# Performance work log

Measured on AMD Instinct MI355X. Metric: run time of the kernel, lower is better.

## Reference

```python
import jax, jax.numpy as jnp
import numpy as np

N, E, G = 50000, 400000, 64          # nodes, edges, graphs in batch
IN_DIM, OUT_DIM = 64, 128
N_ETYPES, N_STEPS = 4, 8


def setup_inputs() -> dict:
    key = jax.random.key(0)
    ks = jax.random.split(key, 13)
    s = 1.0 / np.sqrt(OUT_DIM)
    u = lambda k, shp: jax.random.uniform(k, shp, jnp.float32, -s, s)
    return {
        "node_features": jax.random.normal(ks[0], (N, IN_DIM), jnp.float32),
        "src": jax.random.randint(ks[1], (E,), 0, N),
        "dst": jax.random.randint(ks[2], (E,), 0, N),
        "etype": jax.random.randint(ks[3], (E,), 0, N_ETYPES),
        "graph_ids": jax.random.randint(ks[4], (N,), 0, G),
        "Ws": u(ks[5], (N_ETYPES, OUT_DIM, OUT_DIM)),   # per-edge-type linear
        "bs": u(ks[6], (N_ETYPES, OUT_DIM)),
        "W_ih": u(ks[7], (3 * OUT_DIM, OUT_DIM)),        # GRUCell (r,z,n order)
        "W_hh": u(ks[8], (3 * OUT_DIM, OUT_DIM)),
        "b_ih": u(ks[9], (3 * OUT_DIM,)),
        "b_hh": u(ks[10], (3 * OUT_DIM,)),
        "W_cls": u(ks[11], (1, OUT_DIM + IN_DIM)),
        "b_cls": u(ks[12], (1,)),
    }


def _gru_cell(x, h, W_ih, W_hh, b_ih, b_hh):
    gi = x @ W_ih.T + b_ih
    gh = h @ W_hh.T + b_hh
    ir, iz, i_n = jnp.split(gi, 3, axis=-1)
    hr, hz, h_n = jnp.split(gh, 3, axis=-1)
    r = jax.nn.sigmoid(ir + hr)
    z = jax.nn.sigmoid(iz + hz)
    n = jnp.tanh(i_n + r * h_n)
    return (1.0 - z) * n + z * h


def reference(node_features, src, dst, etype, graph_ids,
              Ws, bs, W_ih, W_hh, b_ih, b_hh, W_cls, b_cls):
    # pad input features to OUT_DIM (GGNN.forward zero_pad)
    h = jnp.concatenate(
        [node_features, jnp.zeros((N, OUT_DIM - IN_DIM), node_features.dtype)], -1)

    def step(h, _):
        # per-edge-type linear transform of all node states: (T, N, D)
        Wh = jnp.einsum('nd,tkd->tnk', h, Ws) + bs[:, None, :]
        msg = Wh[etype, src]                                  # (E, D) gather
        a = jax.ops.segment_sum(msg, dst, num_segments=N)     # scatter-add
        return _gru_cell(a, h, W_ih, W_hh, b_ih, b_hh), None

    h, _ = jax.lax.scan(step, h, None, length=N_STEPS)

    hcat = jnp.concatenate([h, node_features], -1)            # (N, OUT+IN)
    feats = jax.ops.segment_sum(hcat, graph_ids, num_segments=G)  # sum readout
    return jax.nn.sigmoid(feats @ W_cls.T + b_cls)            # (G, 1)
```

## Files before the change

kernel.cpp:

```cpp
#include <hip/hip_runtime.h>
#include <hip/hip_bf16.h>
#include <math.h>


#define NN 50000
#define NE 400000
#define NG 64
#define IND 64
#define OD 128
#define NN4 (NN * 4)
#define RC 8

typedef _Float16 f16x8 __attribute__((ext_vector_type(8)));
typedef _Float16 f16x4 __attribute__((ext_vector_type(4)));
typedef _Float16 f16x2 __attribute__((ext_vector_type(2)));
typedef float f32x4 __attribute__((ext_vector_type(4)));

__device__ inline unsigned short f2h(float x) {
    _Float16 hv = (_Float16)x;
    unsigned short u;
    __builtin_memcpy(&u, &hv, 2);
    return u;
}

__global__ void k_cvtws(const float* __restrict__ Ws, unsigned short* __restrict__ Wcat) {
    int i = blockIdx.x * 256 + threadIdx.x;
    if (i >= 65536) return;
    int o = i >> 9, col = i & 511;
    int t = col >> 7, k = col & 127;
    Wcat[i] = f2h(Ws[t * 16384 + o * 128 + k]);
}

__global__ void k_pack(const float* __restrict__ Wih, const float* __restrict__ Whh,
                       const float* __restrict__ bih, const float* __restrict__ bhh,
                       unsigned short* __restrict__ Wpk, float* __restrict__ bpk) {
    int i = blockIdx.x * 256 + threadIdx.x;
    if (i < 98304) {
        int c = i >> 14, j = i & 16383, o = j >> 7, k = j & 127;
        const float* W = (c & 1) ? Whh : Wih;
        Wpk[i] = f2h(W[((c >> 1) * 128 + o) * 128 + k]);
    }
    if (i < 512) {
        float b;
        if (i < 256) b = bih[i] + bhh[i];
        else if (i < 384) b = bih[i];
        else b = bhh[i - 128];
        bpk[i] = b;
    }
}

__global__ void k_init_h(const float* __restrict__ nf, float* __restrict__ h,
                         unsigned short* __restrict__ hx) {
    int i = blockIdx.x * 256 + threadIdx.x;
    if (i >= NN * OD) return;
    int n = i >> 7, d = i & 127;
    float v = (d < IND) ? nf[n * IND + d] : 0.f;
    h[i] = v;
    hx[(size_t)n * 256 + 128 + d] = f2h(v);
}

__global__ void k_count(const int* __restrict__ dst, const int* __restrict__ et,
                        int* __restrict__ deg4) {
    int e = blockIdx.x * 256 + threadIdx.x;
    if (e < NE) atomicAdd(&deg4[dst[e] * 4 + et[e]], 1);
}

__global__ void k_scan1(const int* __restrict__ deg, int* __restrict__ rowp,
                        int* __restrict__ bsum, int n) {
    __shared__ int buf[1024];
    int tid = threadIdx.x;
    int i = blockIdx.x * 1024 + tid;
    int v = (i < n) ? deg[i] : 0;
    buf[tid] = v;
    __syncthreads();
    for (int off = 1; off < 1024; off <<= 1) {
        int t = (tid >= off) ? buf[tid - off] : 0;
        __syncthreads();
        buf[tid] += t;
        __syncthreads();
    }
    if (i < n) rowp[i + 1] = buf[tid];
    if (tid == 1023) bsum[blockIdx.x] = buf[tid];
}

__global__ void k_scan2(int* __restrict__ bsum, int nb) {
    __shared__ int buf[256];
    int tid = threadIdx.x;
    int v = (tid < nb) ? bsum[tid] : 0;
    buf[tid] = v;
    __syncthreads();
    for (int off = 1; off < 256; off <<= 1) {
        int t = (tid >= off) ? buf[tid - off] : 0;
        __syncthreads();
        buf[tid] += t;
        __syncthreads();
    }
    if (tid < nb) bsum[tid] = buf[tid] - v;
}

__global__ void k_scan3(const int* __restrict__ deg, const int* __restrict__ bsum,
                        int* __restrict__ rowp, int* __restrict__ cursor, int n) {
    int i = blockIdx.x * 256 + threadIdx.x;
    if (i >= n) return;
    int incl = rowp[i + 1] + bsum[i >> 10];
    rowp[i + 1] = incl;
    cursor[i] = incl - deg[i];
    if (i == 0) rowp[0] = 0;
}

__global__ void k_fill(const int* __restrict__ src, const int* __restrict__ dst,
                       const int* __restrict__ et, int* __restrict__ cursor,
                       int* __restrict__ epk) {
    int e = blockIdx.x * 256 + threadIdx.x;
    if (e < NE) {
        int t = et[e];
        int pos = atomicAdd(&cursor[dst[e] * 4 + t], 1);
        epk[pos] = src[e] | (t << 16);
    }
}

__global__ void k_gcount(const int* __restrict__ gid, int* __restrict__ gdeg) {
    __shared__ int c[NG];
    int tid = threadIdx.x;
    if (tid < NG) c[tid] = 0;
    __syncthreads();
    int n = blockIdx.x * 1024 + tid;
    if (n < NN) atomicAdd(&c[gid[n]], 1);
    __syncthreads();
    if (tid < NG && c[tid] > 0) atomicAdd(&gdeg[tid], c[tid]);
}

__global__ void k_gscan(const int* __restrict__ gdeg, int* __restrict__ growp,
                        int* __restrict__ gcur) {
    __shared__ int buf[NG];
    int tid = threadIdx.x;
    int v = gdeg[tid];
    buf[tid] = v;
    __syncthreads();
    for (int off = 1; off < NG; off <<= 1) {
        int t = (tid >= off) ? buf[tid - off] : 0;
        __syncthreads();
        buf[tid] += t;
        __syncthreads();
    }
    growp[tid + 1] = buf[tid];
    gcur[tid] = buf[tid] - v;
    if (tid == 0) growp[0] = 0;
}

__global__ void k_gfill(const int* __restrict__ gid, int* __restrict__ gcur,
                        int* __restrict__ nlist) {
    __shared__ int lcnt[NG];
    __shared__ int lbase[NG];
    int tid = threadIdx.x;
    if (tid < NG) lcnt[tid] = 0;
    __syncthreads();
    int n = blockIdx.x * 1024 + tid;
    int g = -1, rank = 0;
    if (n < NN) { g = gid[n]; rank = atomicAdd(&lcnt[g], 1); }
    __syncthreads();
    if (tid < NG && lcnt[tid] > 0) lbase[tid] = atomicAdd(&gcur[tid], lcnt[tid]);
    __syncthreads();
    if (n < NN) nlist[lbase[g] + rank] = n;
}

__global__ __launch_bounds__(256) void k_agg_gemm(
    const unsigned short* __restrict__ hx,
    const int* __restrict__ rowp4, const int* __restrict__ epk,
    const int* __restrict__ deg4,
    const unsigned short* __restrict__ Wcat,
    const float* __restrict__ bs,
    unsigned short* __restrict__ hxw) {
    __shared__ unsigned short Sh[4 * 32 * 136];
    __shared__ float Bsb[512];

    const int tid = threadIdx.x;
    const int m0 = blockIdx.x * 32;

    Bsb[tid] = bs[tid];
    Bsb[tid + 256] = bs[tid + 256];

    const int r = tid >> 3;
    const int sl = tid & 7;
    const int d0 = sl * 16;
    const int n = m0 + r;

    float a0[16], a1[16], a2[16], a3[16];
#pragma unroll
    for (int k = 0; k < 16; ++k) { a0[k] = 0.f; a1[k] = 0.f; a2[k] = 0.f; a3[k] = 0.f; }

    if (n < NN) {
        int i = rowp4[n * 4], end = rowp4[n * 4 + 4];
        for (; i + 2 <= end; i += 2) {
            int p0 = epk[i], p1 = epk[i + 1];
            const f16x8* r0 = (const f16x8*)&hx[(size_t)(p0 & 0xFFFF) * 256 + 128 + d0];
            const f16x8* r1 = (const f16x8*)&hx[(size_t)(p1 & 0xFFFF) * 256 + 128 + d0];
            f16x8 u0 = r0[0], u1 = r0[1];
            f16x8 v0 = r1[0], v1 = r1[1];
            int e0 = p0 >> 16, e1 = p1 >> 16;
#pragma unroll
            for (int k = 0; k < 8; ++k) {
                float f0 = (float)u0[k], f1 = (float)u1[k];
                float g0 = (float)v0[k], g1 = (float)v1[k];
                a0[k]     += (e0 == 0 ? f0 : 0.f) + (e1 == 0 ? g0 : 0.f);
                a0[8 + k] += (e0 == 0 ? f1 : 0.f) + (e1 == 0 ? g1 : 0.f);
                a1[k]     += (e0 == 1 ? f0 : 0.f) + (e1 == 1 ? g0 : 0.f);
                a1[8 + k] += (e0 == 1 ? f1 : 0.f) + (e1 == 1 ? g1 : 0.f);
                a2[k]     += (e0 == 2 ? f0 : 0.f) + (e1 == 2 ? g0 : 0.f);
                a2[8 + k] += (e0 == 2 ? f1 : 0.f) + (e1 == 2 ? g1 : 0.f);
                a3[k]     += (e0 == 3 ? f0 : 0.f) + (e1 == 3 ? g0 : 0.f);
                a3[8 + k] += (e0 == 3 ? f1 : 0.f) + (e1 == 3 ? g1 : 0.f);
            }
        }
        if (i < end) {
            int p0 = epk[i];
            const f16x8* r0 = (const f16x8*)&hx[(size_t)(p0 & 0xFFFF) * 256 + 128 + d0];
            f16x8 u0 = r0[0], u1 = r0[1];
            int e0 = p0 >> 16;
#pragma unroll
            for (int k = 0; k < 8; ++k) {
                float f0 = (float)u0[k], f1 = (float)u1[k];
                a0[k] += (e0 == 0 ? f0 : 0.f); a0[8 + k] += (e0 == 0 ? f1 : 0.f);
                a1[k] += (e0 == 1 ? f0 : 0.f); a1[8 + k] += (e0 == 1 ? f1 : 0.f);
                a2[k] += (e0 == 2 ? f0 : 0.f); a2[8 + k] += (e0 == 2 ? f1 : 0.f);
                a3[k] += (e0 == 3 ? f0 : 0.f); a3[8 + k] += (e0 == 3 ? f1 : 0.f);
            }
        }
    }

    {
        f16x8 w0, w1;
#pragma unroll
        for (int k = 0; k < 8; ++k) { w0[k] = (_Float16)a0[k]; w1[k] = (_Float16)a0[8 + k]; }
        *(f16x8*)&Sh[0 * 4352 + r * 136 + d0] = w0; *(f16x8*)&Sh[0 * 4352 + r * 136 + d0 + 8] = w1;
#pragma unroll
        for (int k = 0; k < 8; ++k) { w0[k] = (_Float16)a1[k]; w1[k] = (_Float16)a1[8 + k]; }
        *(f16x8*)&Sh[1 * 4352 + r * 136 + d0] = w0; *(f16x8*)&Sh[1 * 4352 + r * 136 + d0 + 8] = w1;
#pragma unroll
        for (int k = 0; k < 8; ++k) { w0[k] = (_Float16)a2[k]; w1[k] = (_Float16)a2[8 + k]; }
        *(f16x8*)&Sh[2 * 4352 + r * 136 + d0] = w0; *(f16x8*)&Sh[2 * 4352 + r * 136 + d0 + 8] = w1;
#pragma unroll
        for (int k = 0; k < 8; ++k) { w0[k] = (_Float16)a3[k]; w1[k] = (_Float16)a3[8 + k]; }
        *(f16x8*)&Sh[3 * 4352 + r * 136 + d0] = w0; *(f16x8*)&Sh[3 * 4352 + r * 136 + d0 + 8] = w1;
    }
    __syncthreads();

    const int lane = tid & 63;
    const int w = tid >> 6;
    const int lr = lane & 15;
    const int q = lane >> 4;
    const int rt = w >> 1;
    const int cts = (w & 1) * 4;

    f32x4 acc[4];
#pragma unroll
    for (int j = 0; j < 4; ++j) acc[j] = (f32x4){0.f, 0.f, 0.f, 0.f};

#pragma unroll
    for (int ks = 0; ks < 16; ++ks) {
        int t = ks >> 2, ksl = ks & 3;
        f16x8 af = *(const f16x8*)&Sh[t * 4352 + (rt * 16 + lr) * 136 + ksl * 32 + q * 8];
#pragma unroll
        for (int j = 0; j < 4; ++j) {
            f16x8 bf = *(const f16x8*)&Wcat[((cts + j) * 16 + lr) * 512 + ks * 32 + q * 8];
            acc[j] = __builtin_amdgcn_mfma_f32_16x16x32_f16(af, bf, acc[j], 0, 0, 0);
        }
    }

    int rowbase = m0 + rt * 16 + q * 4;
#pragma unroll
    for (int rr = 0; rr < 4; ++rr) {
        int n2 = rowbase + rr;
        if (n2 < NN) {
            int4 c = *(const int4*)&deg4[n2 * 4];
            unsigned short* arow = hxw + (size_t)n2 * 256;
#pragma unroll
            for (int j = 0; j < 4; ++j) {
                int col = (cts + j) * 16 + lr;
                float v = acc[j][rr]
                        + c.x * Bsb[col] + c.y * Bsb[128 + col]
                        + c.z * Bsb[256 + col] + c.w * Bsb[384 + col];
                arow[col] = f2h(v);
            }
        }
    }
}

__global__ __launch_bounds__(512) void k_gates_gru(
    const unsigned short* __restrict__ hx,
    const unsigned short* __restrict__ Wpk,
    const float* __restrict__ bpk,
    float* __restrict__ h,
    unsigned short* __restrict__ hxw) {
    __shared__ unsigned short As[64 * 264];
    __shared__ unsigned short Bs[128 * 136];
    __shared__ float Bsb[512];

    const int tid = threadIdx.x;
    const int m0 = blockIdx.x * 64;

    Bsb[tid] = bpk[tid];

    const uint4* H4 = (const uint4*)hx;
#pragma unroll
    for (int it = 0; it < 4; ++it) {
        int i = tid + it * 512;
        int row = i >> 5, qq = i & 31;
        int nn = m0 + row;
        uint4 v = (nn < NN) ? H4[(size_t)nn * 32 + qq] : make_uint4(0u, 0u, 0u, 0u);
        *(uint4*)&As[row * 264 + qq * 8] = v;
    }

    const int lane = tid & 63;
    const int w = tid >> 6;
    const int lr = lane & 15;
    const int q = lane >> 4;
    const int rt = w >> 1;
    const int cts = (w & 1) * 4;

    const uint4* W4 = (const uint4*)Wpk;

    f32x4 accR[4], accZ[4], accI[4], accH[4];
#pragma unroll
    for (int j = 0; j < 4; ++j) {
        accR[j] = (f32x4){0.f, 0.f, 0.f, 0.f};
        accZ[j] = (f32x4){0.f, 0.f, 0.f, 0.f};
        accI[j] = (f32x4){0.f, 0.f, 0.f, 0.f};
        accH[j] = (f32x4){0.f, 0.f, 0.f, 0.f};
    }

#define GCHUNK(C, ACC)                                                              \
    __syncthreads();                                                                \
    _Pragma("unroll")                                                               \
    for (int it = 0; it < 4; ++it) {                                                \
        int i = tid + it * 512;                                                     \
        *(uint4*)&Bs[(i >> 4) * 136 + (i & 15) * 8] = W4[(C) * 2048 + i];           \
    }                                                                               \
    __syncthreads();                                                                \
    _Pragma("unroll")                                                               \
    for (int ks = 0; ks < 4; ++ks) {                                                \
        f16x8 af = *(const f16x8*)&As[(rt * 16 + lr) * 264 + ((C) & 1) * 128        \
                                      + ks * 32 + q * 8];                           \
        _Pragma("unroll")                                                           \
        for (int j = 0; j < 4; ++j) {                                               \
            f16x8 bf = *(const f16x8*)&Bs[((cts + j) * 16 + lr) * 136               \
                                          + ks * 32 + q * 8];                       \
            ACC[j] = __builtin_amdgcn_mfma_f32_16x16x32_f16(af, bf, ACC[j], 0, 0, 0); \
        }                                                                           \
    }

    GCHUNK(0, accR)
    GCHUNK(1, accR)
    GCHUNK(2, accZ)
    GCHUNK(3, accZ)
    GCHUNK(4, accI)
    GCHUNK(5, accH)
#undef GCHUNK

    int rowb = m0 + rt * 16 + q * 4;
#pragma unroll
    for (int rr = 0; rr < 4; ++rr) {
        int n2 = rowb + rr;
        if (n2 < NN) {
            float* hrow = h + (size_t)n2 * OD;
            unsigned short* hbrow = hxw + (size_t)n2 * 256 + 128;
#pragma unroll
            for (int j = 0; j < 4; ++j) {
                int col = (cts + j) * 16 + lr;
                float R = 1.f / (1.f + __expf(-(accR[j][rr] + Bsb[col])));
                float Z = 1.f / (1.f + __expf(-(accZ[j][rr] + Bsb[128 + col])));
                float NV = tanhf(accI[j][rr] + Bsb[256 + col]
                                 + R * (accH[j][rr] + Bsb[384 + col]));
                float hold = hrow[col];
                float hnew = (1.f - Z) * NV + Z * hold;
                hrow[col] = hnew;
                hbrow[col] = f2h(hnew);
            }
        }
    }
}

__global__ void k_readout(const float* __restrict__ h, const float* __restrict__ nf,
                          const int* __restrict__ nlist, const int* __restrict__ growp,
                          float* __restrict__ partial) {
    int g = blockIdx.x >> 3, c = blockIdx.x & (RC - 1);
    int d = threadIdx.x;
    int s = growp[g], e = growp[g + 1], len = e - s;
    int i0 = s + (int)((long long)len * c / RC);
    int i1 = s + (int)((long long)len * (c + 1) / RC);
    float acc = 0.f;
    for (int i = i0; i < i1; ++i) {
        int n = nlist[i];
        acc += (d < OD) ? h[(size_t)n * OD + d] : nf[(size_t)n * IND + (d - OD)];
    }
    partial[(size_t)blockIdx.x * 192 + d] = acc;
}

__global__ void k_reduce(const float* __restrict__ partial, float* __restrict__ feats) {
    int i = blockIdx.x * 256 + threadIdx.x;
    if (i >= NG * 192) return;
    int g = i / 192, d = i % 192;
    float s = 0.f;
    for (int c = 0; c < RC; ++c) s += partial[(size_t)(g * RC + c) * 192 + d];
    feats[i] = s;
}

__global__ void k_final(const float* __restrict__ feats, const float* __restrict__ W_cls,
                        const float* __restrict__ b_cls, float* __restrict__ out) {
    int g = threadIdx.x;
    if (g >= NG) return;
    float acc = b_cls[0];
    for (int d = 0; d < 192; ++d) acc += feats[g * 192 + d] * W_cls[d];
    out[g] = 1.f / (1.f + __expf(-acc));
}

extern "C" void kernel_launch(void* const* d_in, const int* in_sizes, int n_in,
                              void* d_out, int out_size, void* d_ws, size_t ws_size,
                              hipStream_t stream) {
    const float* nf    = (const float*)d_in[0];
    const int*   src   = (const int*)d_in[1];
    const int*   dst   = (const int*)d_in[2];
    const int*   et    = (const int*)d_in[3];
    const int*   gid   = (const int*)d_in[4];
    const float* Ws    = (const float*)d_in[5];
    const float* bs    = (const float*)d_in[6];
    const float* W_ih  = (const float*)d_in[7];
    const float* W_hh  = (const float*)d_in[8];
    const float* b_ih  = (const float*)d_in[9];
    const float* b_hh  = (const float*)d_in[10];
    const float* W_cls = (const float*)d_in[11];
    const float* b_cls = (const float*)d_in[12];
    float* out = (float*)d_out;

    char* ws = (char*)d_ws;
    size_t off = 0;
    auto alloc = [&](size_t bytes) -> void* {
        off = (off + 255) & ~(size_t)255;
        void* p = ws + off;
        off += bytes;
        return p;
    };
    float*          h    = (float*)alloc((size_t)NN * OD * 4);
    unsigned short* hx   = (unsigned short*)alloc((size_t)NN * 256 * 2);
    int*   deg4    = (int*)alloc((size_t)NN4 * 4);
    int*   rowp4   = (int*)alloc((size_t)(NN4 + 1) * 4);
    int*   cursor4 = (int*)alloc((size_t)NN4 * 4);
    int*   epk     = (int*)alloc((size_t)NE * 4);
    int*   bsum    = (int*)alloc(256 * 4);
    int*   gdeg    = (int*)alloc(NG * 4);
    int*   growp   = (int*)alloc((NG + 1) * 4);
    int*   gcur    = (int*)alloc(NG * 4);
    int*   nlist   = (int*)alloc((size_t)NN * 4);
    float* feats   = (float*)alloc((size_t)NG * 192 * 4);
    float* partial = (float*)alloc((size_t)NG * RC * 192 * 4);
    unsigned short* Wcat = (unsigned short*)alloc((size_t)65536 * 2);
    unsigned short* Wpk  = (unsigned short*)alloc((size_t)98304 * 2);
    float*          bpk  = (float*)alloc(512 * 4);
    (void)ws_size; (void)in_sizes; (void)n_in; (void)out_size;

    hipMemsetAsync(deg4, 0, (size_t)NN4 * 4, stream);
    hipMemsetAsync(gdeg, 0, NG * 4, stream);

    k_cvtws<<<(65536 + 255) / 256, 256, 0, stream>>>(Ws, Wcat);
    k_pack<<<(98304 + 255) / 256, 256, 0, stream>>>(W_ih, W_hh, b_ih, b_hh, Wpk, bpk);

    k_init_h<<<(NN * OD + 255) / 256, 256, 0, stream>>>(nf, h, hx);

    k_count<<<(NE + 255) / 256, 256, 0, stream>>>(dst, et, deg4);
    const int nb4 = (NN4 + 1023) / 1024;
    k_scan1<<<nb4, 1024, 0, stream>>>(deg4, rowp4, bsum, NN4);
    k_scan2<<<1, 256, 0, stream>>>(bsum, nb4);
    k_scan3<<<(NN4 + 255) / 256, 256, 0, stream>>>(deg4, bsum, rowp4, cursor4, NN4);
    k_fill<<<(NE + 255) / 256, 256, 0, stream>>>(src, dst, et, cursor4, epk);

    const int nbn = (NN + 1023) / 1024;
    k_gcount<<<nbn, 1024, 0, stream>>>(gid, gdeg);
    k_gscan<<<1, NG, 0, stream>>>(gdeg, growp, gcur);
    k_gfill<<<nbn, 1024, 0, stream>>>(gid, gcur, nlist);

    const int mt32 = (NN + 31) / 32;
    const int mt64 = (NN + 63) / 64;
    for (int s = 0; s < 8; ++s) {
        k_agg_gemm<<<mt32, 256, 0, stream>>>(hx, rowp4, epk, deg4, Wcat, bs, hx);
        k_gates_gru<<<mt64, 512, 0, stream>>>(hx, Wpk, bpk, h, hx);
    }

    k_readout<<<NG * RC, 192, 0, stream>>>(h, nf, nlist, growp, partial);
    k_reduce<<<(NG * 192 + 255) / 256, 256, 0, stream>>>(partial, feats);
    k_final<<<1, 64, 0, stream>>>(feats, W_cls, b_cls, out);
}
```

Measured before the change: 1.133 ms.

## Gather edges wave-per-8-nodes with segmented accumulation keyed by packed dst/type

```diff
diff --git a/kernel.cpp b/kernel.cpp
--- a/kernel.cpp
+++ b/kernel.cpp
@@ -114,8 +114,9 @@
     int e = blockIdx.x * 256 + threadIdx.x;
     if (e < NE) {
         int t = et[e];
-        int pos = atomicAdd(&cursor[dst[e] * 4 + t], 1);
-        epk[pos] = src[e] | (t << 16);
+        int d = dst[e];
+        int pos = atomicAdd(&cursor[d * 4 + t], 1);
+        epk[pos] = src[e] | (t << 16) | ((d & 31) << 18);
     }
 }
 
@@ -176,81 +177,77 @@
 
     const int tid = threadIdx.x;
     const int m0 = blockIdx.x * 32;
+    const int wv = tid >> 6;
+    const int lane = tid & 63;
 
     Bsb[tid] = bs[tid];
     Bsb[tid + 256] = bs[tid + 256];
-
-    const int r = tid >> 3;
-    const int sl = tid & 7;
-    const int d0 = sl * 16;
-    const int n = m0 + r;
-
-    float a0[16], a1[16], a2[16], a3[16];
-#pragma unroll
-    for (int k = 0; k < 16; ++k) { a0[k] = 0.f; a1[k] = 0.f; a2[k] = 0.f; a3[k] = 0.f; }
-
-    if (n < NN) {
-        int i = rowp4[n * 4], end = rowp4[n * 4 + 4];
-        for (; i + 2 <= end; i += 2) {
-            int p0 = epk[i], p1 = epk[i + 1];
-            const f16x8* r0 = (const f16x8*)&hx[(size_t)(p0 & 0xFFFF) * 256 + 128 + d0];
-            const f16x8* r1 = (const f16x8*)&hx[(size_t)(p1 & 0xFFFF) * 256 + 128 + d0];
-            f16x8 u0 = r0[0], u1 = r0[1];
-            f16x8 v0 = r1[0], v1 = r1[1];
-            int e0 = p0 >> 16, e1 = p1 >> 16;
-#pragma unroll
-            for (int k = 0; k < 8; ++k) {
-                float f0 = (float)u0[k], f1 = (float)u1[k];
-                float g0 = (float)v0[k], g1 = (float)v1[k];
-                a0[k]     += (e0 == 0 ? f0 : 0.f) + (e1 == 0 ? g0 : 0.f);
-                a0[8 + k] += (e0 == 0 ? f1 : 0.f) + (e1 == 0 ? g1 : 0.f);
-                a1[k]     += (e0 == 1 ? f0 : 0.f) + (e1 == 1 ? g0 : 0.f);
-                a1[8 + k] += (e0 == 1 ? f1 : 0.f) + (e1 == 1 ? g1 : 0.f);
-                a2[k]     += (e0 == 2 ? f0 : 0.f) + (e1 == 2 ? g0 : 0.f);
-                a2[8 + k] += (e0 == 2 ? f1 : 0.f) + (e1 == 2 ? g1 : 0.f);
-                a3[k]     += (e0 == 3 ? f0 : 0.f) + (e1 == 3 ? g0 : 0.f);
-                a3[8 + k] += (e0 == 3 ? f1 : 0.f) + (e1 == 3 ? g1 : 0.f);
+    {
+        unsigned int* z = (unsigned int*)Sh;
+#pragma unroll
+        for (int i = tid; i < 8704; i += 256) z[i] = 0u;
+    }
+    __syncthreads();
+
+    {
+        const int d2 = lane * 2;
+        int n0 = m0 + wv * 8; if (n0 > NN) n0 = NN;
+        int n1 = n0 + 8;      if (n1 > NN) n1 = NN;
+        const int ebeg = rowp4[n0 * 4];
+        const int eend = rowp4[n1 * 4];
+
+        float a0 = 0.f, a1 = 0.f;
+        int cur = -1;
+        int kq[8];
+        int base = ebeg;
+#pragma unroll
+        for (int j = 0; j < 8; ++j) kq[j] = (base + j < eend) ? epk[base + j] : -1;
+        while (base < eend) {
+            const int nb2 = base + 8;
+            f16x2 v[8];
+#pragma unroll
+            for (int j = 0; j < 8; ++j) {
+                int p = kq[j];
+                if (p >= 0)
+                    v[j] = *(const f16x2*)&hx[(size_t)(p & 0xFFFF) * 256 + 128 + d2];
+                else {
+                    v[j][0] = (_Float16)0.f; v[j][1] = (_Float16)0.f;
+                }
             }
+            int kn[8];
+#pragma unroll
+            for (int j = 0; j < 8; ++j) kn[j] = (nb2 + j < eend) ? epk[nb2 + j] : -1;
+#pragma unroll
+            for (int j = 0; j < 8; ++j) {
+                int p = kq[j];
+                if (p >= 0) {
+                    int key = p >> 16;
+                    if (key != cur) {
+                        if (cur >= 0) {
+                            f16x2 fv; fv[0] = (_Float16)a0; fv[1] = (_Float16)a1;
+                            *(f16x2*)&Sh[(cur & 3) * 4352 + (cur >> 2) * 136 + d2] = fv;
+                        }
+                        cur = key; a0 = 0.f; a1 = 0.f;
+                    }
+                    a0 += (float)v[j][0];
+                    a1 += (float)v[j][1];
+                }
+            }
+#pragma unroll
+            for (int j = 0; j < 8; ++j) kq[j] = kn[j];
+            base = nb2;
         }
-        if (i < end) {
-            int p0 = epk[i];
-            const f16x8* r0 = (const f16x8*)&hx[(size_t)(p0 & 0xFFFF) * 256 + 128 + d0];
-            f16x8 u0 = r0[0], u1 = r0[1];
-            int e0 = p0 >> 16;
-#pragma unroll
-            for (int k = 0; k < 8; ++k) {
-                float f0 = (float)u0[k], f1 = (float)u1[k];
-                a0[k] += (e0 == 0 ? f0 : 0.f); a0[8 + k] += (e0 == 0 ? f1 : 0.f);
-                a1[k] += (e0 == 1 ? f0 : 0.f); a1[8 + k] += (e0 == 1 ? f1 : 0.f);
-                a2[k] += (e0 == 2 ? f0 : 0.f); a2[8 + k] += (e0 == 2 ? f1 : 0.f);
-                a3[k] += (e0 == 3 ? f0 : 0.f); a3[8 + k] += (e0 == 3 ? f1 : 0.f);
-            }
+        if (cur >= 0) {
+            f16x2 fv; fv[0] = (_Float16)a0; fv[1] = (_Float16)a1;
+            *(f16x2*)&Sh[(cur & 3) * 4352 + (cur >> 2) * 136 + d2] = fv;
         }
     }
-
-    {
-        f16x8 w0, w1;
-#pragma unroll
-        for (int k = 0; k < 8; ++k) { w0[k] = (_Float16)a0[k]; w1[k] = (_Float16)a0[8 + k]; }
-        *(f16x8*)&Sh[0 * 4352 + r * 136 + d0] = w0; *(f16x8*)&Sh[0 * 4352 + r * 136 + d0 + 8] = w1;
-#pragma unroll
-        for (int k = 0; k < 8; ++k) { w0[k] = (_Float16)a1[k]; w1[k] = (_Float16)a1[8 + k]; }
-        *(f16x8*)&Sh[1 * 4352 + r * 136 + d0] = w0; *(f16x8*)&Sh[1 * 4352 + r * 136 + d0 + 8] = w1;
-#pragma unroll
-        for (int k = 0; k < 8; ++k) { w0[k] = (_Float16)a2[k]; w1[k] = (_Float16)a2[8 + k]; }
-        *(f16x8*)&Sh[2 * 4352 + r * 136 + d0] = w0; *(f16x8*)&Sh[2 * 4352 + r * 136 + d0 + 8] = w1;
-#pragma unroll
-        for (int k = 0; k < 8; ++k) { w0[k] = (_Float16)a3[k]; w1[k] = (_Float16)a3[8 + k]; }
-        *(f16x8*)&Sh[3 * 4352 + r * 136 + d0] = w0; *(f16x8*)&Sh[3 * 4352 + r * 136 + d0 + 8] = w1;
-    }
-    __syncthreads();
-
-    const int lane = tid & 63;
-    const int w = tid >> 6;
+    __syncthreads();
+
     const int lr = lane & 15;
     const int q = lane >> 4;
-    const int rt = w >> 1;
-    const int cts = (w & 1) * 4;
+    const int rt = wv >> 1;
+    const int cts = (wv & 1) * 4;
 
     f32x4 acc[4];
 #pragma unroll
```

New measurement: 1.203 ms. 6.2% more time.

## Fuse aggregation GEMM and GRU gate kernels into one step kernel with ping-pong buffers

Applied to the files above, without the earlier changes.

```diff
diff --git a/kernel.cpp b/kernel.cpp
--- a/kernel.cpp
+++ b/kernel.cpp
@@ -50,13 +50,13 @@
 }
 
 __global__ void k_init_h(const float* __restrict__ nf, float* __restrict__ h,
-                         unsigned short* __restrict__ hx) {
+                         unsigned short* __restrict__ hb0) {
     int i = blockIdx.x * 256 + threadIdx.x;
     if (i >= NN * OD) return;
     int n = i >> 7, d = i & 127;
     float v = (d < IND) ? nf[n * IND + d] : 0.f;
     h[i] = v;
-    hx[(size_t)n * 256 + 128 + d] = f2h(v);
+    hb0[i] = f2h(v);
 }
 
 __global__ void k_count(const int* __restrict__ dst, const int* __restrict__ et,
@@ -164,21 +164,33 @@
     if (n < NN) nlist[lbase[g] + rank] = n;
 }
 
-__global__ __launch_bounds__(256) void k_agg_gemm(
-    const unsigned short* __restrict__ hx,
+__global__ __launch_bounds__(256) void k_step(
+    const unsigned short* __restrict__ hbc,
+    unsigned short* __restrict__ hbn,
+    float* __restrict__ h,
     const int* __restrict__ rowp4, const int* __restrict__ epk,
     const int* __restrict__ deg4,
     const unsigned short* __restrict__ Wcat,
     const float* __restrict__ bs,
-    unsigned short* __restrict__ hxw) {
+    const unsigned short* __restrict__ Wpk,
+    const float* __restrict__ bpk) {
     __shared__ unsigned short Sh[4 * 32 * 136];
-    __shared__ float Bsb[512];
+    __shared__ unsigned short As[32 * 264];
 
     const int tid = threadIdx.x;
     const int m0 = blockIdx.x * 32;
 
-    Bsb[tid] = bs[tid];
-    Bsb[tid + 256] = bs[tid + 256];
+    {
+        const uint4* Hb4 = (const uint4*)hbc;
+#pragma unroll
+        for (int it = 0; it < 2; ++it) {
+            int i = tid + it * 256;
+            int row = i >> 4, qq = i & 15;
+            int nn = m0 + row;
+            uint4 v = (nn < NN) ? Hb4[(size_t)nn * 16 + qq] : make_uint4(0u, 0u, 0u, 0u);
+            *(uint4*)&As[row * 264 + 128 + qq * 8] = v;
+        }
+    }
 
     const int r = tid >> 3;
     const int sl = tid & 7;
@@ -193,8 +205,8 @@
         int i = rowp4[n * 4], end = rowp4[n * 4 + 4];
         for (; i + 2 <= end; i += 2) {
             int p0 = epk[i], p1 = epk[i + 1];
-            const f16x8* r0 = (const f16x8*)&hx[(size_t)(p0 & 0xFFFF) * 256 + 128 + d0];
-            const f16x8* r1 = (const f16x8*)&hx[(size_t)(p1 & 0xFFFF) * 256 + 128 + d0];
+            const f16x8* r0 = (const f16x8*)&hbc[(size_t)(p0 & 0xFFFF) * 128 + d0];
+            const f16x8* r1 = (const f16x8*)&hbc[(size_t)(p1 & 0xFFFF) * 128 + d0];
             f16x8 u0 = r0[0], u1 = r0[1];
             f16x8 v0 = r1[0], v1 = r1[1];
             int e0 = p0 >> 16, e1 = p1 >> 16;
@@ -214,7 +226,7 @@
         }
         if (i < end) {
             int p0 = epk[i];
-            const f16x8* r0 = (const f16x8*)&hx[(size_t)(p0 & 0xFFFF) * 256 + 128 + d0];
+            const f16x8* r0 = (const f16x8*)&hbc[(size_t)(p0 & 0xFFFF) * 128 + d0];
             f16x8 u0 = r0[0], u1 = r0[1];
             int e0 = p0 >> 16;
 #pragma unroll
@@ -249,75 +261,49 @@
     const int w = tid >> 6;
     const int lr = lane & 15;
     const int q = lane >> 4;
-    const int rt = w >> 1;
-    const int cts = (w & 1) * 4;
-
-    f32x4 acc[4];
-#pragma unroll
-    for (int j = 0; j < 4; ++j) acc[j] = (f32x4){0.f, 0.f, 0.f, 0.f};
-
-#pragma unroll
-    for (int ks = 0; ks < 16; ++ks) {
-        int t = ks >> 2, ksl = ks & 3;
-        f16x8 af = *(const f16x8*)&Sh[t * 4352 + (rt * 16 + lr) * 136 + ksl * 32 + q * 8];
-#pragma unroll
-        for (int j = 0; j < 4; ++j) {
-            f16x8 bf = *(const f16x8*)&Wcat[((cts + j) * 16 + lr) * 512 + ks * 32 + q * 8];
-            acc[j] = __builtin_amdgcn_mfma_f32_16x16x32_f16(af, bf, acc[j], 0, 0, 0);
-        }
-    }
-
-    int rowbase = m0 + rt * 16 + q * 4;
-#pragma unroll
-    for (int rr = 0; rr < 4; ++rr) {
-        int n2 = rowbase + rr;
-        if (n2 < NN) {
-            int4 c = *(const int4*)&deg4[n2 * 4];
-            unsigned short* arow = hxw + (size_t)n2 * 256;
+    const int rt = w & 1;
+    const int cts = (w >> 1) * 4;
+
+    {
+        f32x4 acc[4];
+#pragma unroll
+        for (int j = 0; j < 4; ++j) acc[j] = (f32x4){0.f, 0.f, 0.f, 0.f};
+
+#pragma unroll
+        for (int ks = 0; ks < 16; ++ks) {
+            int t = ks >> 2, ksl = ks & 3;
+            f16x8 af = *(const f16x8*)&Sh[t * 4352 + (rt * 16 + lr) * 136 + ksl * 32 + q * 8];
 #pragma unroll
             for (int j = 0; j < 4; ++j) {
-                int col = (cts + j) * 16 + lr;
-                float v = acc[j][rr]
-                        + c.x * Bsb[col] + c.y * Bsb[128 + col]
-                        + c.z * Bsb[256 + col] + c.w * Bsb[384 + col];
-                arow[col] = f2h(v);
+                f16x8 bf = *(const f16x8*)&Wcat[((cts + j) * 16 + lr) * 512 + ks * 32 + q * 8];
+                acc[j] = __builtin_amdgcn_mfma_f32_16x16x32_f16(af, bf, acc[j], 0, 0, 0);
             }
         }
-    }
-}
-
-__global__ __launch_bounds__(512) void k_gates_gru(
-    const unsigned short* __restrict__ hx,
-    const unsigned short* __restrict__ Wpk,
-    const float* __restrict__ bpk,
-    float* __restrict__ h,
-    unsigned short* __restrict__ hxw) {
-    __shared__ unsigned short As[64 * 264];
-    __shared__ unsigned short Bs[128 * 136];
-    __shared__ float Bsb[512];
-
-    const int tid = threadIdx.x;
-    const int m0 = blockIdx.x * 64;
-
-    Bsb[tid] = bpk[tid];
-
-    const uint4* H4 = (const uint4*)hx;
-#pragma unroll
-    for (int it = 0; it < 4; ++it) {
-        int i = tid + it * 512;
-        int row = i >> 5, qq = i & 31;
-        int nn = m0 + row;
-        uint4 v = (nn < NN) ? H4[(size_t)nn * 32 + qq] : make_uint4(0u, 0u, 0u, 0u);
-        *(uint4*)&As[row * 264 + qq * 8] = v;
-    }
-
-    const int lane = tid & 63;
-    const int w = tid >> 6;
-    const int lr = lane & 15;
-    const int q = lane >> 4;
-    const int rt = w >> 1;
-    const int cts = (w & 1) * 4;
-
+
+        int rowb = rt * 16 + q * 4;
+#pragma unroll
+        for (int rr = 0; rr < 4; ++rr) {
+            int rl = rowb + rr;
+            int n2 = m0 + rl;
+            if (n2 < NN) {
+                int4 c = *(const int4*)&deg4[n2 * 4];
+#pragma unroll
+                for (int j = 0; j < 4; ++j) {
+                    int col = (cts + j) * 16 + lr;
+                    float v = acc[j][rr]
+                            + c.x * bs[col] + c.y * bs[128 + col]
+                            + c.z * bs[256 + col] + c.w * bs[384 + col];
+                    As[rl * 264 + col] = f2h(v);
+                }
+            } else {
+#pragma unroll
+                for (int j = 0; j < 4; ++j)
+                    As[rl * 264 + (cts + j) * 16 + lr] = 0;
+            }
+        }
+    }
+
+    unsigned short* Bs = Sh;
     const uint4* W4 = (const uint4*)Wpk;
 
     f32x4 accR[4], accZ[4], accI[4], accH[4];
@@ -332,8 +318,8 @@
 #define GCHUNK(C, ACC)                                                              \
     __syncthreads();                                                                \
     _Pragma("unroll")                                                               \
-    for (int it = 0; it < 4; ++it) {                                                \
-        int i = tid + it * 512;                                                     \
+    for (int it = 0; it < 8; ++it) {                                                \
+        int i = tid + it * 256;                                                     \
         *(uint4*)&Bs[(i >> 4) * 136 + (i & 15) * 8] = W4[(C) * 2048 + i];           \
     }                                                                               \
     __syncthreads();                                                                \
@@ -363,14 +349,14 @@
         int n2 = rowb + rr;
         if (n2 < NN) {
             float* hrow = h + (size_t)n2 * OD;
-            unsigned short* hbrow = hxw + (size_t)n2 * 256 + 128;
+            unsigned short* hbrow = hbn + (size_t)n2 * OD;
 #pragma unroll
             for (int j = 0; j < 4; ++j) {
                 int col = (cts + j) * 16 + lr;
-                float R = 1.f / (1.f + __expf(-(accR[j][rr] + Bsb[col])));
-                float Z = 1.f / (1.f + __expf(-(accZ[j][rr] + Bsb[128 + col])));
-                float NV = tanhf(accI[j][rr] + Bsb[256 + col]
-                                 + R * (accH[j][rr] + Bsb[384 + col]));
+                float R = 1.f / (1.f + __expf(-(accR[j][rr] + bpk[col])));
+                float Z = 1.f / (1.f + __expf(-(accZ[j][rr] + bpk[128 + col])));
+                float NV = tanhf(accI[j][rr] + bpk[256 + col]
+                                 + R * (accH[j][rr] + bpk[384 + col]));
                 float hold = hrow[col];
                 float hnew = (1.f - Z) * NV + Z * hold;
                 hrow[col] = hnew;
@@ -441,7 +427,8 @@
         return p;
     };
     float*          h    = (float*)alloc((size_t)NN * OD * 4);
-    unsigned short* hx   = (unsigned short*)alloc((size_t)NN * 256 * 2);
+    unsigned short* hb0  = (unsigned short*)alloc((size_t)NN * OD * 2);
+    unsigned short* hb1  = (unsigned short*)alloc((size_t)NN * OD * 2);
     int*   deg4    = (int*)alloc((size_t)NN4 * 4);
     int*   rowp4   = (int*)alloc((size_t)(NN4 + 1) * 4);
     int*   cursor4 = (int*)alloc((size_t)NN4 * 4);
@@ -464,7 +451,7 @@
     k_cvtws<<<(65536 + 255) / 256, 256, 0, stream>>>(Ws, Wcat);
     k_pack<<<(98304 + 255) / 256, 256, 0, stream>>>(W_ih, W_hh, b_ih, b_hh, Wpk, bpk);
 
-    k_init_h<<<(NN * OD + 255) / 256, 256, 0, stream>>>(nf, h, hx);
+    k_init_h<<<(NN * OD + 255) / 256, 256, 0, stream>>>(nf, h, hb0);
 
     k_count<<<(NE + 255) / 256, 256, 0, stream>>>(dst, et, deg4);
     const int nb4 = (NN4 + 1023) / 1024;
@@ -479,10 +466,10 @@
     k_gfill<<<nbn, 1024, 0, stream>>>(gid, gcur, nlist);
 
     const int mt32 = (NN + 31) / 32;
-    const int mt64 = (NN + 63) / 64;
+    unsigned short* hbs[2] = {hb0, hb1};
     for (int s = 0; s < 8; ++s) {
-        k_agg_gemm<<<mt32, 256, 0, stream>>>(hx, rowp4, epk, deg4, Wcat, bs, hx);
-        k_gates_gru<<<mt64, 512, 0, stream>>>(hx, Wpk, bpk, h, hx);
+        k_step<<<mt32, 256, 0, stream>>>(hbs[s & 1], hbs[(s + 1) & 1], h,
+                                         rowp4, epk, deg4, Wcat, bs, Wpk, bpk);
     }
 
     k_readout<<<NG * RC, 192, 0, stream>>>(h, nf, nlist, growp, partial);
```

Result: slower. 1.267 ms (+11.9%).
